# Kernel optimization log

Measured on AMD Instinct MI355X. Metric: run time of the kernel, lower is better.

The kernel has to match this reference:

```python
import jax, jax.numpy as jnp
import numpy as np
import math

HIDDEN = 1024
HEADS = 16
HEAD_DIM = HIDDEN // HEADS


def setup_inputs() -> dict:
    key = jax.random.key(0)
    ks = jax.random.split(key, 9)
    s = 1.0 / math.sqrt(HIDDEN)
    x = jax.random.normal(ks[0], (4, 2048, HIDDEN), dtype=jnp.float32)
    Wq = jax.random.uniform(ks[1], (HIDDEN, HIDDEN), jnp.float32, -s, s)
    bq = jax.random.uniform(ks[2], (HIDDEN,), jnp.float32, -s, s)
    Wk = jax.random.uniform(ks[3], (HIDDEN, HIDDEN), jnp.float32, -s, s)
    bk = jax.random.uniform(ks[4], (HIDDEN,), jnp.float32, -s, s)
    Wv = jax.random.uniform(ks[5], (HIDDEN, HIDDEN), jnp.float32, -s, s)
    bv = jax.random.uniform(ks[6], (HIDDEN,), jnp.float32, -s, s)
    Wo = jax.random.uniform(ks[7], (HIDDEN, HIDDEN), jnp.float32, -s, s)
    bo = jax.random.uniform(ks[8], (HIDDEN,), jnp.float32, -s, s)
    return {"x": x, "Wq": Wq, "bq": bq, "Wk": Wk, "bk": bk,
            "Wv": Wv, "bv": bv, "Wo": Wo, "bo": bo}


def reference(x, Wq, bq, Wk, bk, Wv, bv, Wo, bo):
    B, T, D = x.shape
    H, Hd = HEADS, HEAD_DIM
    scale = 1.0 / math.sqrt(Hd)
    # projections (torch Linear: y = x @ W.T + b)
    q = (x @ Wq.T + bq).reshape(B, T, H, Hd).transpose(0, 2, 1, 3)  # [B,H,T,Hd]
    k = (x @ Wk.T + bk).reshape(B, T, H, Hd).transpose(0, 2, 1, 3)
    v = (x @ Wv.T + bv).reshape(B, T, H, Hd).transpose(0, 2, 1, 3)
    scores = jnp.einsum("bhqd,bhkd->bhqk", q, k) * scale  # [B,H,T,T]
    attn = jax.nn.softmax(scores, axis=-1)
    out = jnp.einsum("bhqk,bhkd->bhqd", attn, v)  # [B,H,T,Hd]
    out = out.transpose(0, 2, 1, 3).reshape(B, T, D)
    out = out @ Wo.T + bo
    return out.mean(axis=1)  # [B, D]
```

## Files before the change

### kernel.cpp

```cpp
#include <hip/hip_runtime.h>
#include <stdint.h>

#define HIDDEN 1024
#define HEADS 16
#define HEAD_DIM 64
#define BATCH 4
#define SEQ 2048
#define NTOK (BATCH * SEQ)

typedef __attribute__((ext_vector_type(8))) short bf16x8;
typedef __attribute__((ext_vector_type(4))) float floatx4;
typedef __attribute__((ext_vector_type(16))) float floatx16;

#define SCALE_Q 0.18033688011112042f

__device__ __forceinline__ unsigned short f2bf(float f) {
    union { float f; unsigned u; } x; x.f = f;
    unsigned r = x.u + 0x7fffu + ((x.u >> 16) & 1u);
    return (unsigned short)(r >> 16);
}

__device__ __forceinline__ float fast_exp2(float x) {
#if __has_builtin(__builtin_amdgcn_exp2f)
    return __builtin_amdgcn_exp2f(x);
#else
    return exp2f(x);
#endif
}

typedef __attribute__((address_space(3))) unsigned int lds_u32;
typedef const __attribute__((address_space(1))) unsigned int gl_u32;

__device__ __forceinline__ void async_cp16(const void* g, void* l) {
#if __has_builtin(__builtin_amdgcn_global_load_lds)
    __builtin_amdgcn_global_load_lds((gl_u32*)g, (lds_u32*)l, 16, 0, 0);
#else
    *(uint4*)((char*)l + (threadIdx.x & 63) * 16) = *(const uint4*)g;
#endif
}

__global__ __launch_bounds__(256) void conv_all(
    const float* __restrict__ x, const float* __restrict__ Wq,
    const float* __restrict__ Wk, const float* __restrict__ Wv,
    unsigned short* __restrict__ x_bf, unsigned short* __restrict__ wq_bf,
    unsigned short* __restrict__ wk_bf, unsigned short* __restrict__ wv_bf,
    float* __restrict__ accp) {
    const int blk = blockIdx.x, tid = threadIdx.x;
    const float* src;
    unsigned short* dst;
    size_t i;
    if (blk < 8192) {
        src = x; dst = x_bf; i = (size_t)blk * 256 + tid;
        if (blk < 16) accp[blk * 256 + tid] = 0.0f;
    } else {
        int r = blk - 8192;
        int s = r >> 10;
        src = (s == 0) ? Wq : (s == 1) ? Wk : Wv;
        dst = (s == 0) ? wq_bf : (s == 1) ? wk_bf : wv_bf;
        i = (size_t)(r & 1023) * 256 + tid;
    }
    float4 v = *(const float4*)(src + 4 * i);
    unsigned short o[4];
    o[0] = f2bf(v.x); o[1] = f2bf(v.y); o[2] = f2bf(v.z); o[3] = f2bf(v.w);
    *(ushort4*)(dst + 4 * i) = *(ushort4*)o;
}

__global__ __launch_bounds__(256, 3) void qkv_gemm(
    const unsigned short* __restrict__ X,
    const unsigned short* __restrict__ W0, const unsigned short* __restrict__ W1,
    const unsigned short* __restrict__ W2,
    const float* __restrict__ b0, const float* __restrict__ b1,
    const float* __restrict__ b2,
    unsigned short* __restrict__ O0, unsigned short* __restrict__ O1,
    unsigned short* __restrict__ O2) {
    __shared__ __align__(16) char smem[34816];
    unsigned short* tbuf = (unsigned short*)smem;

    const int id = blockIdx.x;
    const int mb = id & 63, nzb = id >> 6;
    const int z = nzb >> 3, nz = nzb & 7;
    const int m0 = mb * 128;
    const unsigned short* W = (z == 0) ? W0 : (z == 1) ? W1 : W2;
    const float* bias       = (z == 0) ? b0 : (z == 1) ? b1 : b2;

    const int tid = threadIdx.x, lane = tid & 63, wave = tid >> 6;
    const int wm = (wave & 1) * 64, wn = (wave >> 1) * 64;

    const int srow = lane >> 2;
    const int sxc = ((lane & 3) ^ (srow & 3)) * 8;
    const unsigned short* ga[2];
    const unsigned short* gb[2];
#pragma unroll
    for (int j = 0; j < 2; ++j) {
        ga[j] = X + (size_t)(m0 + wave * 32 + j * 16 + srow) * HIDDEN + sxc;
        gb[j] = W + (size_t)(nz * 128 + wave * 32 + j * 16 + srow) * HIDDEN + sxc;
    }

    floatx4 acc[4][4];
#pragma unroll
    for (int tm = 0; tm < 4; ++tm)
#pragma unroll
        for (int tn = 0; tn < 4; ++tn)
#pragma unroll
            for (int r = 0; r < 4; ++r) acc[tm][tn][r] = 0.f;

#pragma unroll
    for (int j = 0; j < 2; ++j) {
        async_cp16(ga[j], smem + wave * 2048 + j * 1024);
        async_cp16(gb[j], smem + 16384 + wave * 2048 + j * 1024);
        ga[j] += 32; gb[j] += 32;
    }
    __syncthreads();

    const int fr = (lane & 15) * 64 + (((lane >> 4) ^ (lane & 3)) * 16);
    for (int kt = 0; kt < 32; ++kt) {
        const int cur = kt & 1;
        if (kt < 31) {
#pragma unroll
            for (int j = 0; j < 2; ++j) {
                async_cp16(ga[j], smem + (cur ^ 1) * 8192 + wave * 2048 + j * 1024);
                async_cp16(gb[j], smem + 16384 + (cur ^ 1) * 8192 + wave * 2048 + j * 1024);
                ga[j] += 32; gb[j] += 32;
            }
        }
        const char* Ab = smem + cur * 8192;
        const char* Bb = smem + 16384 + cur * 8192;
        bf16x8 af[4], bfr[4];
#pragma unroll
        for (int t = 0; t < 4; ++t) {
            af[t]  = *(bf16x8*)(Ab + (wm + t * 16) * 64 + fr);
            bfr[t] = *(bf16x8*)(Bb + (wn + t * 16) * 64 + fr);
        }
#pragma unroll
        for (int tm = 0; tm < 4; ++tm)
#pragma unroll
            for (int tn = 0; tn < 4; ++tn)
                acc[tm][tn] = __builtin_amdgcn_mfma_f32_16x16x32_bf16(af[tm], bfr[tn], acc[tm][tn], 0, 0, 0);
        if (kt < 31) __syncthreads();
    }

    const int col = lane & 15, rbase = (lane >> 4) * 4;
    __syncthreads();
    if (z == 2) {
#pragma unroll
        for (int tm = 0; tm < 4; ++tm)
#pragma unroll
            for (int tn = 0; tn < 4; ++tn) {
                const int dr = wn + tn * 16 + col;
                const float bs = bias[nz * 128 + dr];
                const int mi0 = wm + tm * 16 + rbase;
                const int mip = (mi0 & ~12) | ((mi0 & 4) << 1) | ((mi0 & 8) >> 1);
                unsigned short vals[4];
#pragma unroll
                for (int r = 0; r < 4; ++r) vals[r] = f2bf(acc[tm][tn][r] + bs);
                *(ushort4*)&tbuf[dr * 136 + mip] = *(ushort4*)vals;
            }
        __syncthreads();
        const int dr = tid >> 1, seg = tid & 1;
        const int hh = nz * 2 + (dr >> 6), dd = dr & 63;
        const int bb = m0 >> 11, tb = (m0 & (SEQ - 1)) >> 7;
        unsigned short* dst = O2 + (((size_t)bb * HEADS + hh) * HEAD_DIM + dd) * SEQ
                                 + tb * 128 + seg * 64;
        const unsigned short* srcl = &tbuf[dr * 136 + seg * 64];
#pragma unroll
        for (int i = 0; i < 8; ++i)
            *(uint4*)(dst + i * 8) = *(const uint4*)(srcl + i * 8);
    } else {
        unsigned short* O = (z == 0) ? O0 : O1;
        const float sc = (z == 0) ? SCALE_Q : 1.0f;
#pragma unroll
        for (int tm = 0; tm < 4; ++tm)
#pragma unroll
            for (int tn = 0; tn < 4; ++tn) {
                const int nn = wn + tn * 16 + col;
                const float bs = bias[nz * 128 + nn];
                const int mi0 = wm + tm * 16 + rbase;
#pragma unroll
                for (int r = 0; r < 4; ++r)
                    tbuf[(mi0 + r) * 136 + nn] = f2bf((acc[tm][tn][r] + bs) * sc);
            }
        __syncthreads();
        const int r = tid >> 1, seg = tid & 1;
        unsigned short* dst = O + (size_t)(m0 + r) * HIDDEN + nz * 128 + seg * 64;
        const unsigned short* srcl = &tbuf[r * 136 + seg * 64];
#pragma unroll
        for (int i = 0; i < 8; ++i)
            *(uint4*)(dst + i * 8) = *(const uint4*)(srcl + i * 8);
    }
}

__global__ __launch_bounds__(256, 4) void attn_mfma(
    const unsigned short* __restrict__ Q, const unsigned short* __restrict__ K,
    const unsigned short* __restrict__ Vt, float* __restrict__ accp) {
    __shared__ unsigned short Klds[2][4096];
    __shared__ unsigned short Vlds[2][4096];

    const int tid = threadIdx.x, lane = tid & 63, wave = tid >> 6;
    const int lq = lane & 31, g2 = lane >> 5;

    const int f = blockIdx.x;
    const int bh = (f & 7) * 8 + ((f >> 3) & 7);
    const int qc = f >> 6;
    const int b = bh >> 4, h = bh & 15;

    bf16x8 qfrag[4];
    {
        const size_t qb = ((size_t)(b * SEQ + qc * 128 + wave * 32 + lq)) * HIDDEN
                          + h * HEAD_DIM + g2 * 8;
#pragma unroll
        for (int ds = 0; ds < 4; ++ds) qfrag[ds] = *(const bf16x8*)&Q[qb + ds * 16];
    }

    const unsigned short* kg[2];
    const unsigned short* vg[2];
    {
        const int kr = lane >> 3;
        const int kc = ((lane & 7) ^ kr) * 8;
#pragma unroll
        for (int j = 0; j < 2; ++j)
            kg[j] = K + ((size_t)(b * SEQ + wave * 16 + j * 8 + kr)) * HIDDEN + h * HEAD_DIM + kc;
#pragma unroll
        for (int j = 0; j < 2; ++j) {
            const int dl = wave * 16 + j * 8 + (lane >> 3);
            const int cc = ((lane & 7) ^ (dl & 7)) * 8;
            vg[j] = Vt + ((size_t)bh * HEAD_DIM + dl) * SEQ + cc;
        }
    }

    floatx16 oacc[2], lacc;
#pragma unroll
    for (int r = 0; r < 16; ++r) { oacc[0][r] = 0.f; oacc[1][r] = 0.f; lacc[r] = 0.f; }

    bf16x8 ones;
    {
        union { bf16x8 v; unsigned u[4]; } o;
        o.u[0] = o.u[1] = o.u[2] = o.u[3] = 0x3F803F80u;
        ones = o.v;
    }

#pragma unroll
    for (int j = 0; j < 2; ++j) {
        async_cp16(kg[j], (char*)Klds[0] + (wave * 16 + j * 8) * 128);
        async_cp16(vg[j], (char*)Vlds[0] + (wave * 16 + j * 8) * 128);
        kg[j] += 64 * HIDDEN; vg[j] += 64;
    }
    __syncthreads();

    for (int it = 0; it < 32; ++it) {
        const int cur = it & 1;
        if (it < 31) {
#pragma unroll
            for (int j = 0; j < 2; ++j) {
                async_cp16(kg[j], (char*)Klds[cur ^ 1] + (wave * 16 + j * 8) * 128);
                async_cp16(vg[j], (char*)Vlds[cur ^ 1] + (wave * 16 + j * 8) * 128);
                kg[j] += 64 * HIDDEN; vg[j] += 64;
            }
        }
#pragma unroll
        for (int s32 = 0; s32 < 2; ++s32) {
            const int rr = s32 * 32 + lq;
            bf16x8 kf[4];
#pragma unroll
            for (int ds = 0; ds < 4; ++ds)
                kf[ds] = *(bf16x8*)((char*)Klds[cur] + rr * 128 + (((g2 + 2 * ds) ^ (lq & 7)) * 16));

            floatx16 sacc;
#pragma unroll
            for (int r = 0; r < 16; ++r) sacc[r] = 0.f;
#pragma unroll
            for (int ds = 0; ds < 4; ++ds)
                sacc = __builtin_amdgcn_mfma_f32_32x32x16_bf16(kf[ds], qfrag[ds], sacc, 0, 0, 0);

            unsigned pk[8];
#pragma unroll
            for (int j = 0; j < 8; ++j) {
                union { float f; unsigned u; } plo, phi;
                plo.f = fast_exp2(sacc[2 * j]);
                phi.f = fast_exp2(sacc[2 * j + 1]);
                pk[j] = __builtin_amdgcn_perm(phi.u, plo.u, 0x07060302u);
            }
#pragma unroll
            for (int ks2 = 0; ks2 < 2; ++ks2) {
                const int s = s32 * 2 + ks2;
                bf16x8 vf[2];
#pragma unroll
                for (int nf = 0; nf < 2; ++nf) {
                    const int d = nf * 32 + lq;
                    const int c = (2 * s + g2) ^ (d & 7);
                    vf[nf] = *(bf16x8*)((char*)Vlds[cur] + d * 128 + c * 16);
                }
                union { uint4 u; bf16x8 v; } af;
                af.u.x = pk[4 * ks2];
                af.u.y = pk[4 * ks2 + 1];
                af.u.z = pk[4 * ks2 + 2];
                af.u.w = pk[4 * ks2 + 3];
#pragma unroll
                for (int nf = 0; nf < 2; ++nf)
                    oacc[nf] = __builtin_amdgcn_mfma_f32_32x32x16_bf16(af.v, vf[nf], oacc[nf], 0, 0, 0);
                lacc = __builtin_amdgcn_mfma_f32_32x32x16_bf16(af.v, ones, lacc, 0, 0, 0);
            }
        }
        if (it < 31) __syncthreads();
    }

#pragma unroll
    for (int nf = 0; nf < 2; ++nf) {
        float v = 0.f;
#pragma unroll
        for (int r = 0; r < 16; ++r) v += oacc[nf][r] / lacc[r];
        v += __shfl_xor(v, 32, 64);
        if (lane < 32)
            atomicAdd(&accp[b * HIDDEN + h * HEAD_DIM + nf * 32 + lq], v);
    }
}

__global__ __launch_bounds__(256) void out_proj(const float* __restrict__ acc,
                                                const float* __restrict__ Wo,
                                                const float* __restrict__ bo,
                                                float* __restrict__ out) {
    __shared__ float red[256];
    const int n = blockIdx.x * 64 + (threadIdx.x & 63);
    const int ks = threadIdx.x >> 6;
    const int b = blockIdx.y;
    const float* wr = Wo + (size_t)n * HIDDEN + ks * 256;
    const float* ar = acc + b * HIDDEN + ks * 256;
    float s = 0.f;
#pragma unroll 8
    for (int k = 0; k < 256; k += 4) {
        float4 w = *(const float4*)(wr + k);
        float4 a = *(const float4*)(ar + k);
        s += w.x * a.x + w.y * a.y + w.z * a.z + w.w * a.w;
    }
    red[threadIdx.x] = s;
    __syncthreads();
    if (threadIdx.x < 64) {
        float t = red[threadIdx.x] + red[threadIdx.x + 64]
                + red[threadIdx.x + 128] + red[threadIdx.x + 192];
        out[b * HIDDEN + n] = t * (1.0f / (float)SEQ) + bo[n];
    }
}

extern "C" void kernel_launch(void* const* d_in, const int* in_sizes, int n_in,
                              void* d_out, int out_size, void* d_ws, size_t ws_size,
                              hipStream_t stream) {
    const float* x  = (const float*)d_in[0];
    const float* Wq = (const float*)d_in[1];
    const float* bq = (const float*)d_in[2];
    const float* Wk = (const float*)d_in[3];
    const float* bk = (const float*)d_in[4];
    const float* Wv = (const float*)d_in[5];
    const float* bv = (const float*)d_in[6];
    const float* Wo = (const float*)d_in[7];
    const float* bo = (const float*)d_in[8];
    float* out = (float*)d_out;

    char* ws = (char*)d_ws;
    unsigned short* x_bf  = (unsigned short*)(ws);
    unsigned short* wq_bf = (unsigned short*)(ws + 16777216);
    unsigned short* wk_bf = (unsigned short*)(ws + 18874368);
    unsigned short* wv_bf = (unsigned short*)(ws + 20971520);
    unsigned short* q_bf  = (unsigned short*)(ws + 23068672);
    unsigned short* k_bf  = (unsigned short*)(ws + 39845888);
    unsigned short* vt_bf = (unsigned short*)(ws + 56623104);
    float*          accp  = (float*)(ws + 73400320);

    conv_all<<<dim3(8192 + 3072), dim3(256), 0, stream>>>(
        x, Wq, Wk, Wv, x_bf, wq_bf, wk_bf, wv_bf, accp);

    qkv_gemm<<<dim3(1536), dim3(256), 0, stream>>>(
        x_bf, wq_bf, wk_bf, wv_bf, bq, bk, bv, q_bf, k_bf, vt_bf);

    attn_mfma<<<dim3(1024), dim3(256), 0, stream>>>(q_bf, k_bf, vt_bf, accp);

    out_proj<<<dim3(16, BATCH), dim3(256), 0, stream>>>(accp, Wo, bo, out);
}
```

Baseline: 250.8 us.

## Load K/V fragments directly from global memory and compute row sums with VALU

The attention kernel drops its double-buffered LDS staging of K and V tiles and the block-wide barriers. Each wave now loads its MFMA operand fragments straight from global memory. The row-sum MFMA against a ones vector is replaced by scalar accumulation of the bf16-rounded probabilities, with a small LDS exchange to line up the sums with the accumulator layout. This removes LDS traffic, barriers and one MFMA per step, but every wave fetches the same K/V data independently through L1/L2 with less coalesced access. It also adds per-element VALU work, and the LDS exchange relies on a waitcnt without a barrier.

Result: slower. 405.5 us (+61.7%).

```diff
diff --git a/kernel.cpp b/kernel.cpp
--- a/kernel.cpp
+++ b/kernel.cpp
@@ -192,8 +192,7 @@
 __global__ __launch_bounds__(256, 4) void attn_mfma(
     const unsigned short* __restrict__ Q, const unsigned short* __restrict__ K,
     const unsigned short* __restrict__ Vt, float* __restrict__ accp) {
-    __shared__ unsigned short Klds[2][4096];
-    __shared__ unsigned short Vlds[2][4096];
+    __shared__ float lbuf[4][32];
 
     const int tid = threadIdx.x, lane = tid & 63, wave = tid >> 6;
     const int lq = lane & 31, g2 = lane >> 5;
@@ -211,58 +210,32 @@
         for (int ds = 0; ds < 4; ++ds) qfrag[ds] = *(const bf16x8*)&Q[qb + ds * 16];
     }
 
-    const unsigned short* kg[2];
-    const unsigned short* vg[2];
-    {
-        const int kr = lane >> 3;
-        const int kc = ((lane & 7) ^ kr) * 8;
-#pragma unroll
-        for (int j = 0; j < 2; ++j)
-            kg[j] = K + ((size_t)(b * SEQ + wave * 16 + j * 8 + kr)) * HIDDEN + h * HEAD_DIM + kc;
-#pragma unroll
-        for (int j = 0; j < 2; ++j) {
-            const int dl = wave * 16 + j * 8 + (lane >> 3);
-            const int cc = ((lane & 7) ^ (dl & 7)) * 8;
-            vg[j] = Vt + ((size_t)bh * HEAD_DIM + dl) * SEQ + cc;
-        }
-    }
-
-    floatx16 oacc[2], lacc;
-#pragma unroll
-    for (int r = 0; r < 16; ++r) { oacc[0][r] = 0.f; oacc[1][r] = 0.f; lacc[r] = 0.f; }
-
-    bf16x8 ones;
-    {
-        union { bf16x8 v; unsigned u[4]; } o;
-        o.u[0] = o.u[1] = o.u[2] = o.u[3] = 0x3F803F80u;
-        ones = o.v;
-    }
-
-#pragma unroll
-    for (int j = 0; j < 2; ++j) {
-        async_cp16(kg[j], (char*)Klds[0] + (wave * 16 + j * 8) * 128);
-        async_cp16(vg[j], (char*)Vlds[0] + (wave * 16 + j * 8) * 128);
-        kg[j] += 64 * HIDDEN; vg[j] += 64;
-    }
-    __syncthreads();
+    const unsigned short* kp = K + ((size_t)(b * SEQ + lq)) * HIDDEN + h * HEAD_DIM + g2 * 8;
+    const unsigned short* vp0 = Vt + ((size_t)(bh * HEAD_DIM) + lq) * SEQ + g2 * 8;
+    const unsigned short* vp1 = vp0 + (size_t)32 * SEQ;
+
+    floatx16 oacc[2];
+#pragma unroll
+    for (int r = 0; r < 16; ++r) { oacc[0][r] = 0.f; oacc[1][r] = 0.f; }
+    float lsum = 0.f;
 
     for (int it = 0; it < 32; ++it) {
-        const int cur = it & 1;
-        if (it < 31) {
-#pragma unroll
-            for (int j = 0; j < 2; ++j) {
-                async_cp16(kg[j], (char*)Klds[cur ^ 1] + (wave * 16 + j * 8) * 128);
-                async_cp16(vg[j], (char*)Vlds[cur ^ 1] + (wave * 16 + j * 8) * 128);
-                kg[j] += 64 * HIDDEN; vg[j] += 64;
-            }
-        }
+        const unsigned short* kwin = kp + (size_t)it * 64 * HIDDEN;
+        const unsigned short* vw0 = vp0 + it * 64;
+        const unsigned short* vw1 = vp1 + it * 64;
 #pragma unroll
         for (int s32 = 0; s32 < 2; ++s32) {
-            const int rr = s32 * 32 + lq;
-            bf16x8 kf[4];
+            bf16x8 kf[4], vf[2][2];
+            const unsigned short* kr = kwin + (size_t)s32 * 32 * HIDDEN;
 #pragma unroll
             for (int ds = 0; ds < 4; ++ds)
-                kf[ds] = *(bf16x8*)((char*)Klds[cur] + rr * 128 + (((g2 + 2 * ds) ^ (lq & 7)) * 16));
+                kf[ds] = *(const bf16x8*)(kr + ds * 16);
+#pragma unroll
+            for (int ks2 = 0; ks2 < 2; ++ks2) {
+                const int ch = (s32 * 2 + ks2) * 16;
+                vf[ks2][0] = *(const bf16x8*)(vw0 + ch);
+                vf[ks2][1] = *(const bf16x8*)(vw1 + ch);
+            }
 
             floatx16 sacc;
 #pragma unroll
@@ -278,17 +251,14 @@
                 plo.f = fast_exp2(sacc[2 * j]);
                 phi.f = fast_exp2(sacc[2 * j + 1]);
                 pk[j] = __builtin_amdgcn_perm(phi.u, plo.u, 0x07060302u);
-            }
+                union { unsigned u; float f; } tlo, thi;
+                tlo.u = pk[j] << 16;
+                thi.u = pk[j] & 0xFFFF0000u;
+                lsum += tlo.f + thi.f;
+            }
+
 #pragma unroll
             for (int ks2 = 0; ks2 < 2; ++ks2) {
-                const int s = s32 * 2 + ks2;
-                bf16x8 vf[2];
-#pragma unroll
-                for (int nf = 0; nf < 2; ++nf) {
-                    const int d = nf * 32 + lq;
-                    const int c = (2 * s + g2) ^ (d & 7);
-                    vf[nf] = *(bf16x8*)((char*)Vlds[cur] + d * 128 + c * 16);
-                }
                 union { uint4 u; bf16x8 v; } af;
                 af.u.x = pk[4 * ks2];
                 af.u.y = pk[4 * ks2 + 1];
@@ -296,18 +266,31 @@
                 af.u.w = pk[4 * ks2 + 3];
 #pragma unroll
                 for (int nf = 0; nf < 2; ++nf)
-                    oacc[nf] = __builtin_amdgcn_mfma_f32_32x32x16_bf16(af.v, vf[nf], oacc[nf], 0, 0, 0);
-                lacc = __builtin_amdgcn_mfma_f32_32x32x16_bf16(af.v, ones, lacc, 0, 0, 0);
+                    oacc[nf] = __builtin_amdgcn_mfma_f32_32x32x16_bf16(af.v, vf[ks2][nf], oacc[nf], 0, 0, 0);
             }
         }
-        if (it < 31) __syncthreads();
-    }
-
+    }
+
+    lsum += __shfl_xor(lsum, 32, 64);
+    if (lane < 32) lbuf[wave][lq] = lsum;
+    __builtin_amdgcn_s_waitcnt(0);
+    float4 l4[4];
+#pragma unroll
+    for (int c = 0; c < 4; ++c)
+        l4[c] = *(float4*)&lbuf[wave][c * 8 + g2 * 4];
+    float inv[16];
+#pragma unroll
+    for (int c = 0; c < 4; ++c) {
+        inv[4 * c + 0] = 1.0f / l4[c].x;
+        inv[4 * c + 1] = 1.0f / l4[c].y;
+        inv[4 * c + 2] = 1.0f / l4[c].z;
+        inv[4 * c + 3] = 1.0f / l4[c].w;
+    }
 #pragma unroll
     for (int nf = 0; nf < 2; ++nf) {
         float v = 0.f;
 #pragma unroll
-        for (int r = 0; r < 16; ++r) v += oacc[nf][r] / lacc[r];
+        for (int r = 0; r < 16; ++r) v += oacc[nf][r] * inv[r];
         v += __shfl_xor(v, 32, 64);
         if (lane < 32)
             atomicAdd(&accp[b * HIDDEN + h * HEAD_DIM + nf * 32 + lq], v);
```

## Double query rows per attention wave and replace ones-MFMA row sums with VALU sums

Applied to the files above, without the earlier changes.

Each wave now processes two 32-row query groups (256 query rows per block), so every K/V tile loaded into LDS and every K/V fragment read from LDS is reused across twice as many queries, and the grid halves to 512 blocks. The softmax denominator was computed with an extra MFMA against a ones vector. It is now accumulated with scalar adds of the bf16-rounded probabilities, then exchanged through a small LDS buffer to line up with the MFMA output layout. In exchange, register pressure rises (occupancy hint lowered from 4 to 3 blocks) and the grid has fewer blocks, which may leave CUs underfilled.

Measured after the change: 285.5 us. 1.14x slower.

```diff
diff --git a/kernel.cpp b/kernel.cpp
--- a/kernel.cpp
+++ b/kernel.cpp
@@ -189,11 +189,12 @@
     }
 }
 
-__global__ __launch_bounds__(256, 4) void attn_mfma(
+__global__ __launch_bounds__(256, 3) void attn_mfma(
     const unsigned short* __restrict__ Q, const unsigned short* __restrict__ K,
     const unsigned short* __restrict__ Vt, float* __restrict__ accp) {
     __shared__ unsigned short Klds[2][4096];
     __shared__ unsigned short Vlds[2][4096];
+    __shared__ float lbuf[4][2][32];
 
     const int tid = threadIdx.x, lane = tid & 63, wave = tid >> 6;
     const int lq = lane & 31, g2 = lane >> 5;
@@ -203,12 +204,13 @@
     const int qc = f >> 6;
     const int b = bh >> 4, h = bh & 15;
 
-    bf16x8 qfrag[4];
-    {
-        const size_t qb = ((size_t)(b * SEQ + qc * 128 + wave * 32 + lq)) * HIDDEN
+    bf16x8 qfrag[2][4];
+#pragma unroll
+    for (int g = 0; g < 2; ++g) {
+        const size_t qb = ((size_t)(b * SEQ + qc * 256 + wave * 64 + g * 32 + lq)) * HIDDEN
                           + h * HEAD_DIM + g2 * 8;
 #pragma unroll
-        for (int ds = 0; ds < 4; ++ds) qfrag[ds] = *(const bf16x8*)&Q[qb + ds * 16];
+        for (int ds = 0; ds < 4; ++ds) qfrag[g][ds] = *(const bf16x8*)&Q[qb + ds * 16];
     }
 
     const unsigned short* kg[2];
@@ -227,16 +229,12 @@
         }
     }
 
-    floatx16 oacc[2], lacc;
-#pragma unroll
-    for (int r = 0; r < 16; ++r) { oacc[0][r] = 0.f; oacc[1][r] = 0.f; lacc[r] = 0.f; }
-
-    bf16x8 ones;
-    {
-        union { bf16x8 v; unsigned u[4]; } o;
-        o.u[0] = o.u[1] = o.u[2] = o.u[3] = 0x3F803F80u;
-        ones = o.v;
-    }
+    floatx16 oacc[2][2];
+#pragma unroll
+    for (int g = 0; g < 2; ++g)
+#pragma unroll
+        for (int r = 0; r < 16; ++r) { oacc[g][0][r] = 0.f; oacc[g][1][r] = 0.f; }
+    float lsum[2] = {0.f, 0.f};
 
 #pragma unroll
     for (int j = 0; j < 2; ++j) {
@@ -263,51 +261,76 @@
 #pragma unroll
             for (int ds = 0; ds < 4; ++ds)
                 kf[ds] = *(bf16x8*)((char*)Klds[cur] + rr * 128 + (((g2 + 2 * ds) ^ (lq & 7)) * 16));
-
-            floatx16 sacc;
-#pragma unroll
-            for (int r = 0; r < 16; ++r) sacc[r] = 0.f;
-#pragma unroll
-            for (int ds = 0; ds < 4; ++ds)
-                sacc = __builtin_amdgcn_mfma_f32_32x32x16_bf16(kf[ds], qfrag[ds], sacc, 0, 0, 0);
-
-            unsigned pk[8];
-#pragma unroll
-            for (int j = 0; j < 8; ++j) {
-                union { float f; unsigned u; } plo, phi;
-                plo.f = fast_exp2(sacc[2 * j]);
-                phi.f = fast_exp2(sacc[2 * j + 1]);
-                pk[j] = __builtin_amdgcn_perm(phi.u, plo.u, 0x07060302u);
-            }
-#pragma unroll
-            for (int ks2 = 0; ks2 < 2; ++ks2) {
-                const int s = s32 * 2 + ks2;
-                bf16x8 vf[2];
+            bf16x8 vf[2][2];
+#pragma unroll
+            for (int ks2 = 0; ks2 < 2; ++ks2)
 #pragma unroll
                 for (int nf = 0; nf < 2; ++nf) {
                     const int d = nf * 32 + lq;
-                    const int c = (2 * s + g2) ^ (d & 7);
-                    vf[nf] = *(bf16x8*)((char*)Vlds[cur] + d * 128 + c * 16);
+                    const int c = (2 * (s32 * 2 + ks2) + g2) ^ (d & 7);
+                    vf[ks2][nf] = *(bf16x8*)((char*)Vlds[cur] + d * 128 + c * 16);
                 }
-                union { uint4 u; bf16x8 v; } af;
-                af.u.x = pk[4 * ks2];
-                af.u.y = pk[4 * ks2 + 1];
-                af.u.z = pk[4 * ks2 + 2];
-                af.u.w = pk[4 * ks2 + 3];
-#pragma unroll
-                for (int nf = 0; nf < 2; ++nf)
-                    oacc[nf] = __builtin_amdgcn_mfma_f32_32x32x16_bf16(af.v, vf[nf], oacc[nf], 0, 0, 0);
-                lacc = __builtin_amdgcn_mfma_f32_32x32x16_bf16(af.v, ones, lacc, 0, 0, 0);
+#pragma unroll
+            for (int g = 0; g < 2; ++g) {
+                floatx16 sacc;
+#pragma unroll
+                for (int r = 0; r < 16; ++r) sacc[r] = 0.f;
+#pragma unroll
+                for (int ds = 0; ds < 4; ++ds)
+                    sacc = __builtin_amdgcn_mfma_f32_32x32x16_bf16(kf[ds], qfrag[g][ds], sacc, 0, 0, 0);
+
+                unsigned pk[8];
+#pragma unroll
+                for (int j = 0; j < 8; ++j) {
+                    union { float f; unsigned u; } plo, phi;
+                    plo.f = fast_exp2(sacc[2 * j]);
+                    phi.f = fast_exp2(sacc[2 * j + 1]);
+                    pk[j] = __builtin_amdgcn_perm(phi.u, plo.u, 0x07060302u);
+                    union { unsigned u; float f; } tlo, thi;
+                    tlo.u = pk[j] << 16;
+                    thi.u = pk[j] & 0xFFFF0000u;
+                    lsum[g] += tlo.f + thi.f;
+                }
+#pragma unroll
+                for (int ks2 = 0; ks2 < 2; ++ks2) {
+                    union { uint4 u; bf16x8 v; } af;
+                    af.u.x = pk[4 * ks2];
+                    af.u.y = pk[4 * ks2 + 1];
+                    af.u.z = pk[4 * ks2 + 2];
+                    af.u.w = pk[4 * ks2 + 3];
+#pragma unroll
+                    for (int nf = 0; nf < 2; ++nf)
+                        oacc[g][nf] = __builtin_amdgcn_mfma_f32_32x32x16_bf16(af.v, vf[ks2][nf], oacc[g][nf], 0, 0, 0);
+                }
             }
         }
         if (it < 31) __syncthreads();
     }
 
+#pragma unroll
+    for (int g = 0; g < 2; ++g) {
+        float ls = lsum[g] + __shfl_xor(lsum[g], 32, 64);
+        if (lane < 32) lbuf[wave][g][lq] = ls;
+    }
+    __builtin_amdgcn_s_waitcnt(0);
+    float inv[2][16];
+#pragma unroll
+    for (int g = 0; g < 2; ++g)
+#pragma unroll
+        for (int c = 0; c < 4; ++c) {
+            float4 l4 = *(float4*)&lbuf[wave][g][c * 8 + g2 * 4];
+            inv[g][4 * c + 0] = 1.0f / l4.x;
+            inv[g][4 * c + 1] = 1.0f / l4.y;
+            inv[g][4 * c + 2] = 1.0f / l4.z;
+            inv[g][4 * c + 3] = 1.0f / l4.w;
+        }
 #pragma unroll
     for (int nf = 0; nf < 2; ++nf) {
         float v = 0.f;
 #pragma unroll
-        for (int r = 0; r < 16; ++r) v += oacc[nf][r] / lacc[r];
+        for (int g = 0; g < 2; ++g)
+#pragma unroll
+            for (int r = 0; r < 16; ++r) v += oacc[g][nf][r] * inv[g][r];
         v += __shfl_xor(v, 32, 64);
         if (lane < 32)
             atomicAdd(&accp[b * HIDDEN + h * HEAD_DIM + nf * 32 + lq], v);
@@ -370,7 +393,7 @@
     qkv_gemm<<<dim3(1536), dim3(256), 0, stream>>>(
         x_bf, wq_bf, wk_bf, wv_bf, bq, bk, bv, q_bf, k_bf, vt_bf);
 
-    attn_mfma<<<dim3(1024), dim3(256), 0, stream>>>(q_bf, k_bf, vt_bf, accp);
+    attn_mfma<<<dim3(512), dim3(256), 0, stream>>>(q_bf, k_bf, vt_bf, accp);
 
     out_proj<<<dim3(16, BATCH), dim3(256), 0, stream>>>(accp, Wo, bo, out);
 }
```
